# Performance work log

Measured on AMD Instinct MI355X. Metric: run time of the kernel, lower is better.

## Reference

```python
import jax, jax.numpy as jnp
import numpy as np

N_GRAPH = 1024
NODES_PER_GRAPH = 512
TOTAL_NODES = N_GRAPH * NODES_PER_GRAPH  # 524288
D_FEAT = 128
EPS = 1e-06


def setup_inputs() -> dict:
    key = jax.random.key(0)
    k1, k2, k3, k4 = jax.random.split(key, 4)
    x = jax.random.normal(k1, (TOTAL_NODES, D_FEAT), dtype=jnp.float32)
    # per-graph node counts; sum(n_node) == TOTAL_NODES (equal-size graphs)
    n_node = jnp.full((N_GRAPH,), NODES_PER_GRAPH, dtype=jnp.int32)
    mean_scale = jax.random.uniform(k2, (D_FEAT,), dtype=jnp.float32)
    scale = jax.random.uniform(k3, (D_FEAT,), dtype=jnp.float32)
    bias = jax.random.normal(k4, (D_FEAT,), dtype=jnp.float32)
    return {"x": x, "n_node": n_node, "mean_scale": mean_scale, "scale": scale, "bias": bias}


def reference(x, n_node, mean_scale, scale, bias):
    n_graph = n_node.shape[0]
    total_nodes = x.shape[0]
    node_graph_idx = jnp.repeat(jnp.arange(n_graph), n_node, axis=0,
                                total_repeat_length=total_nodes)  # [N]
    ones = jnp.ones((total_nodes, 1), dtype=x.dtype)
    counts = jax.ops.segment_sum(ones, node_graph_idx, n_graph)  # [G,1]
    # per-graph mean, broadcast back to nodes
    mean_g = jax.ops.segment_sum(x, node_graph_idx, n_graph) / counts  # [G,D]
    mean_n = jnp.repeat(mean_g, n_node, axis=0, total_repeat_length=total_nodes)
    # NOTE: faithful to source - the mean is scaled by mean_scale BEFORE both
    # the centering and the variance computation.
    mean_n = mean_n * mean_scale
    y = x - mean_n
    var_g = jax.ops.segment_sum((x - mean_n) ** 2, node_graph_idx, n_graph) / counts
    var_n = jnp.repeat(var_g, n_node, axis=0, total_repeat_length=total_nodes)
    mul = jax.lax.rsqrt(var_n + EPS) * scale
    y = y * mul + bias
    return y.astype(x.dtype)
```

## Files before the change

kernel.cpp:

```cpp
#include <hip/hip_runtime.h>

#define D_FEAT 128
#define F4 (D_FEAT / 4)
#define BLOCK 1024
#define FAST_NODES 512
#define PER_THREAD (FAST_NODES * F4 / BLOCK)
#define EPS 1e-6f

__global__ __launch_bounds__(BLOCK, 4) void graphnorm_kernel(
    const float* __restrict__ x,
    const int* __restrict__ n_node,
    const float* __restrict__ mean_scale,
    const float* __restrict__ scale,
    const float* __restrict__ bias,
    float* __restrict__ y,
    int n_graph)
{
    const int g    = blockIdx.x;
    const int t    = threadIdx.x;
    const int lane = t & 63;
    const int wave = t >> 6;
    const int grp  = t & 31;
    const int nsub = t >> 5;

    __shared__ int    s_int[16];
    __shared__ float4 s_sum[16][32];
    __shared__ float4 s_sq [16][32];
    __shared__ float4 s_a[32];
    __shared__ float4 s_b[32];
    __shared__ int    s_off;

    int my = 0;
    for (int i = t; i < g; i += BLOCK) my += n_node[i];
    #pragma unroll
    for (int o = 32; o; o >>= 1) my += __shfl_down(my, o);
    if (lane == 0) s_int[wave] = my;
    __syncthreads();
    if (t == 0) {
        int tot = 0;
        #pragma unroll
        for (int w = 0; w < 16; w++) tot += s_int[w];
        s_off = tot;
    }
    __syncthreads();
    const int   node0 = s_off;
    const int   cnt   = n_node[g];
    const float inv   = 1.0f / (float)cnt;

    const float4* __restrict__ xg = (const float4*)x + (size_t)node0 * F4;
    float4*       __restrict__ yg = (float4*)y       + (size_t)node0 * F4;

    float4 sum = make_float4(0.f, 0.f, 0.f, 0.f);
    float4 sq  = make_float4(0.f, 0.f, 0.f, 0.f);

    float4 v[PER_THREAD];
    const bool fast = (cnt == FAST_NODES);

    if (fast) {
        #pragma unroll
        for (int i = 0; i < PER_THREAD; i++) {
            const int node = nsub + 32 * i;
            v[i] = xg[(size_t)node * F4 + grp];
            sum.x += v[i].x; sum.y += v[i].y; sum.z += v[i].z; sum.w += v[i].w;
            sq.x  += v[i].x * v[i].x; sq.y += v[i].y * v[i].y;
            sq.z  += v[i].z * v[i].z; sq.w += v[i].w * v[i].w;
        }
    } else {
        for (int node = nsub; node < cnt; node += 32) {
            float4 val = xg[(size_t)node * F4 + grp];
            sum.x += val.x; sum.y += val.y; sum.z += val.z; sum.w += val.w;
            sq.x  += val.x * val.x; sq.y += val.y * val.y;
            sq.z  += val.z * val.z; sq.w += val.w * val.w;
        }
    }

    sum.x += __shfl_down(sum.x, 32); sum.y += __shfl_down(sum.y, 32);
    sum.z += __shfl_down(sum.z, 32); sum.w += __shfl_down(sum.w, 32);
    sq.x  += __shfl_down(sq.x, 32);  sq.y  += __shfl_down(sq.y, 32);
    sq.z  += __shfl_down(sq.z, 32);  sq.w  += __shfl_down(sq.w, 32);
    if (lane < 32) { s_sum[wave][lane] = sum; s_sq[wave][lane] = sq; }
    __syncthreads();

    if (t < 32) {
        float4 S = make_float4(0.f, 0.f, 0.f, 0.f);
        float4 Q = make_float4(0.f, 0.f, 0.f, 0.f);
        #pragma unroll
        for (int w = 0; w < 16; w++) {
            float4 a4 = s_sum[w][t];
            float4 b4 = s_sq[w][t];
            S.x += a4.x; S.y += a4.y; S.z += a4.z; S.w += a4.w;
            Q.x += b4.x; Q.y += b4.y; Q.z += b4.z; Q.w += b4.w;
        }
        const float4 ms = ((const float4*)mean_scale)[t];
        const float4 sc = ((const float4*)scale)[t];
        const float4 bs = ((const float4*)bias)[t];

        float4 A, B;
        {
            float mean = S.x * inv, m = mean * ms.x;
            float var  = Q.x * inv - 2.f * m * mean + m * m;
            A.x = rsqrtf(var + EPS) * sc.x; B.x = bs.x - m * A.x;
        }
        {
            float mean = S.y * inv, m = mean * ms.y;
            float var  = Q.y * inv - 2.f * m * mean + m * m;
            A.y = rsqrtf(var + EPS) * sc.y; B.y = bs.y - m * A.y;
        }
        {
            float mean = S.z * inv, m = mean * ms.z;
            float var  = Q.z * inv - 2.f * m * mean + m * m;
            A.z = rsqrtf(var + EPS) * sc.z; B.z = bs.z - m * A.z;
        }
        {
            float mean = S.w * inv, m = mean * ms.w;
            float var  = Q.w * inv - 2.f * m * mean + m * m;
            A.w = rsqrtf(var + EPS) * sc.w; B.w = bs.w - m * A.w;
        }
        s_a[t] = A; s_b[t] = B;
    }
    __syncthreads();

    const float4 a = s_a[grp];
    const float4 b = s_b[grp];

    if (fast) {
        #pragma unroll
        for (int i = 0; i < PER_THREAD; i++) {
            const int node = nsub + 32 * i;
            float4 r;
            r.x = v[i].x * a.x + b.x;
            r.y = v[i].y * a.y + b.y;
            r.z = v[i].z * a.z + b.z;
            r.w = v[i].w * a.w + b.w;
            yg[(size_t)node * F4 + grp] = r;
        }
    } else {
        for (int node = nsub; node < cnt; node += 32) {
            float4 val = xg[(size_t)node * F4 + grp];
            float4 r;
            r.x = val.x * a.x + b.x;
            r.y = val.y * a.y + b.y;
            r.z = val.z * a.z + b.z;
            r.w = val.w * a.w + b.w;
            yg[(size_t)node * F4 + grp] = r;
        }
    }
}

extern "C" void kernel_launch(void* const* d_in, const int* in_sizes, int n_in,
                              void* d_out, int out_size, void* d_ws, size_t ws_size,
                              hipStream_t stream) {
    const float* x          = (const float*)d_in[0];
    const int*   n_node     = (const int*)d_in[1];
    const float* mean_scale = (const float*)d_in[2];
    const float* scale      = (const float*)d_in[3];
    const float* bias       = (const float*)d_in[4];
    float*       y          = (float*)d_out;

    const int n_graph = in_sizes[1];

    graphnorm_kernel<<<n_graph, BLOCK, 0, stream>>>(
        x, n_node, mean_scale, scale, bias, y, n_graph);
}
```

Before: 452.6 us.

## Split graph norm into separate stats and apply kernels with reverse-order apply

Replaces the single fused kernel, which held each graph's rows in registers, with a stats kernel that computes per-graph scale and shift and an apply kernel that rereads x. Both use 512-thread blocks with higher occupancy, and the apply pass walks graphs in reverse so recently read data may still be in cache. Coefficients go to workspace, or into the output buffer when no workspace is given. The cost is a second full read of x plus an extra launch.

```diff
diff --git a/kernel.cpp b/kernel.cpp
--- a/kernel.cpp
+++ b/kernel.cpp
@@ -1,91 +1,94 @@
 #include <hip/hip_runtime.h>
 
 #define D_FEAT 128
-#define F4 (D_FEAT / 4)
-#define BLOCK 1024
-#define FAST_NODES 512
-#define PER_THREAD (FAST_NODES * F4 / BLOCK)
-#define EPS 1e-6f
-
-__global__ __launch_bounds__(BLOCK, 4) void graphnorm_kernel(
-    const float* __restrict__ x,
-    const int* __restrict__ n_node,
-    const float* __restrict__ mean_scale,
-    const float* __restrict__ scale,
-    const float* __restrict__ bias,
-    float* __restrict__ y,
-    int n_graph)
+#define F4     (D_FEAT / 4)
+#define BLOCK  512
+#define EPS    1e-6f
+
+__device__ __forceinline__ int graph_offset(const int* __restrict__ n_node,
+                                            int g, int t)
 {
-    const int g    = blockIdx.x;
-    const int t    = threadIdx.x;
-    const int lane = t & 63;
-    const int wave = t >> 6;
-    const int grp  = t & 31;
-    const int nsub = t >> 5;
-
-    __shared__ int    s_int[16];
-    __shared__ float4 s_sum[16][32];
-    __shared__ float4 s_sq [16][32];
-    __shared__ float4 s_a[32];
-    __shared__ float4 s_b[32];
-    __shared__ int    s_off;
-
+    __shared__ int s_red[8];
+    __shared__ int s_off;
     int my = 0;
     for (int i = t; i < g; i += BLOCK) my += n_node[i];
     #pragma unroll
     for (int o = 32; o; o >>= 1) my += __shfl_down(my, o);
-    if (lane == 0) s_int[wave] = my;
+    if ((t & 63) == 0) s_red[t >> 6] = my;
     __syncthreads();
     if (t == 0) {
         int tot = 0;
         #pragma unroll
-        for (int w = 0; w < 16; w++) tot += s_int[w];
+        for (int w = 0; w < 8; w++) tot += s_red[w];
         s_off = tot;
     }
     __syncthreads();
-    const int   node0 = s_off;
-    const int   cnt   = n_node[g];
-    const float inv   = 1.0f / (float)cnt;
+    return s_off;
+}
+
+__global__ __launch_bounds__(BLOCK, 8) void gn_stats(
+    const float* __restrict__ x,
+    const int*   __restrict__ n_node,
+    const float* __restrict__ mean_scale,
+    const float* __restrict__ scale,
+    const float* __restrict__ bias,
+    float*       __restrict__ y,
+    float4*      __restrict__ coef,
+    int n_graph, int mode)
+{
+    const int g    = blockIdx.x;
+    const int t    = threadIdx.x;
+    const int grp  = t & 31;
+    const int nsub = t >> 5;
+    const int wave = t >> 6;
+    const int lane = t & 63;
+
+    const int node0 = graph_offset(n_node, g, t);
+    const int cnt   = n_node[g];
 
     const float4* __restrict__ xg = (const float4*)x + (size_t)node0 * F4;
-    float4*       __restrict__ yg = (float4*)y       + (size_t)node0 * F4;
 
     float4 sum = make_float4(0.f, 0.f, 0.f, 0.f);
     float4 sq  = make_float4(0.f, 0.f, 0.f, 0.f);
 
-    float4 v[PER_THREAD];
-    const bool fast = (cnt == FAST_NODES);
-
-    if (fast) {
-        #pragma unroll
-        for (int i = 0; i < PER_THREAD; i++) {
-            const int node = nsub + 32 * i;
-            v[i] = xg[(size_t)node * F4 + grp];
-            sum.x += v[i].x; sum.y += v[i].y; sum.z += v[i].z; sum.w += v[i].w;
-            sq.x  += v[i].x * v[i].x; sq.y += v[i].y * v[i].y;
-            sq.z  += v[i].z * v[i].z; sq.w += v[i].w * v[i].w;
-        }
-    } else {
-        for (int node = nsub; node < cnt; node += 32) {
-            float4 val = xg[(size_t)node * F4 + grp];
-            sum.x += val.x; sum.y += val.y; sum.z += val.z; sum.w += val.w;
-            sq.x  += val.x * val.x; sq.y += val.y * val.y;
-            sq.z  += val.z * val.z; sq.w += val.w * val.w;
-        }
+    int node = nsub;
+    for (; node + 48 < cnt; node += 64) {
+        float4 v0 = xg[(size_t)(node     ) * F4 + grp];
+        float4 v1 = xg[(size_t)(node + 16) * F4 + grp];
+        float4 v2 = xg[(size_t)(node + 32) * F4 + grp];
+        float4 v3 = xg[(size_t)(node + 48) * F4 + grp];
+        sum.x += v0.x + v1.x + v2.x + v3.x;
+        sum.y += v0.y + v1.y + v2.y + v3.y;
+        sum.z += v0.z + v1.z + v2.z + v3.z;
+        sum.w += v0.w + v1.w + v2.w + v3.w;
+        sq.x += v0.x*v0.x + v1.x*v1.x + v2.x*v2.x + v3.x*v3.x;
+        sq.y += v0.y*v0.y + v1.y*v1.y + v2.y*v2.y + v3.y*v3.y;
+        sq.z += v0.z*v0.z + v1.z*v1.z + v2.z*v2.z + v3.z*v3.z;
+        sq.w += v0.w*v0.w + v1.w*v1.w + v2.w*v2.w + v3.w*v3.w;
+    }
+    for (; node < cnt; node += 16) {
+        float4 v0 = xg[(size_t)node * F4 + grp];
+        sum.x += v0.x; sum.y += v0.y; sum.z += v0.z; sum.w += v0.w;
+        sq.x += v0.x*v0.x; sq.y += v0.y*v0.y;
+        sq.z += v0.z*v0.z; sq.w += v0.w*v0.w;
     }
 
     sum.x += __shfl_down(sum.x, 32); sum.y += __shfl_down(sum.y, 32);
     sum.z += __shfl_down(sum.z, 32); sum.w += __shfl_down(sum.w, 32);
     sq.x  += __shfl_down(sq.x, 32);  sq.y  += __shfl_down(sq.y, 32);
     sq.z  += __shfl_down(sq.z, 32);  sq.w  += __shfl_down(sq.w, 32);
+
+    __shared__ float4 s_sum[8][32];
+    __shared__ float4 s_sq [8][32];
     if (lane < 32) { s_sum[wave][lane] = sum; s_sq[wave][lane] = sq; }
     __syncthreads();
 
     if (t < 32) {
+        const float inv = 1.0f / (float)cnt;
         float4 S = make_float4(0.f, 0.f, 0.f, 0.f);
         float4 Q = make_float4(0.f, 0.f, 0.f, 0.f);
         #pragma unroll
-        for (int w = 0; w < 16; w++) {
+        for (int w = 0; w < 8; w++) {
             float4 a4 = s_sum[w][t];
             float4 b4 = s_sq[w][t];
             S.x += a4.x; S.y += a4.y; S.z += a4.z; S.w += a4.w;
@@ -116,34 +119,79 @@
             float var  = Q.w * inv - 2.f * m * mean + m * m;
             A.w = rsqrtf(var + EPS) * sc.w; B.w = bs.w - m * A.w;
         }
-        s_a[t] = A; s_b[t] = B;
+
+        if (mode == 0) {
+            coef[(size_t)g * 32 + t]             = A;
+            coef[(size_t)(n_graph + g) * 32 + t] = B;
+        } else if (cnt >= 2) {
+            float4* ygc = (float4*)y + (size_t)node0 * F4;
+            ygc[t]      = A;
+            ygc[32 + t] = B;
+        }
+    }
+}
+
+__global__ __launch_bounds__(BLOCK, 8) void gn_apply(
+    const float* __restrict__ x,
+    const int*   __restrict__ n_node,
+    float*       __restrict__ y,
+    const float4* __restrict__ coef,
+    int n_graph, int mode)
+{
+    const int g    = n_graph - 1 - blockIdx.x;
+    const int t    = threadIdx.x;
+    const int grp  = t & 31;
+    const int nsub = t >> 5;
+
+    const int node0 = graph_offset(n_node, g, t);
+    const int cnt   = n_node[g];
+
+    __shared__ float4 s_a[32];
+    __shared__ float4 s_b[32];
+    if (mode == 0) {
+        if (t < 32)      s_a[t]      = coef[(size_t)g * 32 + t];
+        else if (t < 64) s_b[t - 32] = coef[(size_t)(n_graph + g) * 32 + (t - 32)];
+    } else {
+        const float4* ygc = (const float4*)y + (size_t)node0 * F4;
+        if (t < 64) {
+            if (t < 32) s_a[t]      = ygc[t];
+            else        s_b[t - 32] = ygc[t];
+        }
     }
     __syncthreads();
 
     const float4 a = s_a[grp];
     const float4 b = s_b[grp];
 
-    if (fast) {
-        #pragma unroll
-        for (int i = 0; i < PER_THREAD; i++) {
-            const int node = nsub + 32 * i;
-            float4 r;
-            r.x = v[i].x * a.x + b.x;
-            r.y = v[i].y * a.y + b.y;
-            r.z = v[i].z * a.z + b.z;
-            r.w = v[i].w * a.w + b.w;
-            yg[(size_t)node * F4 + grp] = r;
-        }
-    } else {
-        for (int node = nsub; node < cnt; node += 32) {
-            float4 val = xg[(size_t)node * F4 + grp];
-            float4 r;
-            r.x = val.x * a.x + b.x;
-            r.y = val.y * a.y + b.y;
-            r.z = val.z * a.z + b.z;
-            r.w = val.w * a.w + b.w;
-            yg[(size_t)node * F4 + grp] = r;
-        }
+    const float4* __restrict__ xg = (const float4*)x + (size_t)node0 * F4;
+    float4*       __restrict__ yg = (float4*)y       + (size_t)node0 * F4;
+
+    int node = nsub;
+    for (; node + 48 < cnt; node += 64) {
+        float4 v0 = xg[(size_t)(node     ) * F4 + grp];
+        float4 v1 = xg[(size_t)(node + 16) * F4 + grp];
+        float4 v2 = xg[(size_t)(node + 32) * F4 + grp];
+        float4 v3 = xg[(size_t)(node + 48) * F4 + grp];
+        float4 r0, r1, r2, r3;
+        r0.x = fmaf(v0.x, a.x, b.x); r0.y = fmaf(v0.y, a.y, b.y);
+        r0.z = fmaf(v0.z, a.z, b.z); r0.w = fmaf(v0.w, a.w, b.w);
+        r1.x = fmaf(v1.x, a.x, b.x); r1.y = fmaf(v1.y, a.y, b.y);
+        r1.z = fmaf(v1.z, a.z, b.z); r1.w = fmaf(v1.w, a.w, b.w);
+        r2.x = fmaf(v2.x, a.x, b.x); r2.y = fmaf(v2.y, a.y, b.y);
+        r2.z = fmaf(v2.z, a.z, b.z); r2.w = fmaf(v2.w, a.w, b.w);
+        r3.x = fmaf(v3.x, a.x, b.x); r3.y = fmaf(v3.y, a.y, b.y);
+        r3.z = fmaf(v3.z, a.z, b.z); r3.w = fmaf(v3.w, a.w, b.w);
+        yg[(size_t)(node     ) * F4 + grp] = r0;
+        yg[(size_t)(node + 16) * F4 + grp] = r1;
+        yg[(size_t)(node + 32) * F4 + grp] = r2;
+        yg[(size_t)(node + 48) * F4 + grp] = r3;
+    }
+    for (; node < cnt; node += 16) {
+        float4 v0 = xg[(size_t)node * F4 + grp];
+        float4 r0;
+        r0.x = fmaf(v0.x, a.x, b.x); r0.y = fmaf(v0.y, a.y, b.y);
+        r0.z = fmaf(v0.z, a.z, b.z); r0.w = fmaf(v0.w, a.w, b.w);
+        yg[(size_t)node * F4 + grp] = r0;
     }
 }
 
@@ -159,6 +207,13 @@
 
     const int n_graph = in_sizes[1];
 
-    graphnorm_kernel<<<n_graph, BLOCK, 0, stream>>>(
-        x, n_node, mean_scale, scale, bias, y, n_graph);
-}
+    const size_t need = (size_t)n_graph * D_FEAT * 2 * sizeof(float);
+    int     mode = 1;
+    float4* coef = nullptr;
+    if (d_ws != nullptr && ws_size >= need) { mode = 0; coef = (float4*)d_ws; }
+
+    gn_stats<<<n_graph, BLOCK, 0, stream>>>(
+        x, n_node, mean_scale, scale, bias, y, coef, n_graph, mode);
+    gn_apply<<<n_graph, BLOCK, 0, stream>>>(
+        x, n_node, y, coef, n_graph, mode);
+}
```

Result: slower. 523.2 us (+15.6%).

## Make graphnorm persistent with software-pipelined store of previous graph

Applied to the files above, without the earlier changes.

Replaces the one-block-per-graph launch with a persistent grid of 256 blocks that loop over graphs in a strided order, keeping a running node offset. Inside each iteration, the normalized stores for the previous graph are interleaved with the loads for the next graph, so reads and writes overlap instead of alternating per block. This cuts block launch overhead and tail effects. In exchange it adds per-iteration prefix sums and barriers, and the 256-block grid may leave some CUs with fewer resident waves.

```diff
diff --git a/kernel.cpp b/kernel.cpp
--- a/kernel.cpp
+++ b/kernel.cpp
@@ -1,78 +1,46 @@
 #include <hip/hip_runtime.h>
 
 #define D_FEAT 128
-#define F4 (D_FEAT / 4)
-#define BLOCK 1024
+#define F4     (D_FEAT / 4)
+#define BLOCK  1024
+#define GRID   256
 #define FAST_NODES 512
-#define PER_THREAD (FAST_NODES * F4 / BLOCK)
-#define EPS 1e-6f
-
-__global__ __launch_bounds__(BLOCK, 4) void graphnorm_kernel(
-    const float* __restrict__ x,
-    const int* __restrict__ n_node,
-    const float* __restrict__ mean_scale,
-    const float* __restrict__ scale,
-    const float* __restrict__ bias,
-    float* __restrict__ y,
-    int n_graph)
+#define PT     (FAST_NODES * F4 / BLOCK)
+#define EPS    1e-6f
+
+__device__ __forceinline__ int coop_sum(const int* __restrict__ n_node,
+                                        int lo, int hi, int t)
 {
-    const int g    = blockIdx.x;
-    const int t    = threadIdx.x;
-    const int lane = t & 63;
-    const int wave = t >> 6;
-    const int grp  = t & 31;
-    const int nsub = t >> 5;
-
-    __shared__ int    s_int[16];
+    __shared__ int s_red[16];
+    __shared__ int s_tot;
+    int my = 0;
+    for (int i = lo + t; i < hi; i += BLOCK) my += n_node[i];
+    #pragma unroll
+    for (int o = 32; o; o >>= 1) my += __shfl_down(my, o);
+    if ((t & 63) == 0) s_red[t >> 6] = my;
+    __syncthreads();
+    if (t == 0) {
+        int tot = 0;
+        #pragma unroll
+        for (int w = 0; w < 16; w++) tot += s_red[w];
+        s_tot = tot;
+    }
+    __syncthreads();
+    return s_tot;
+}
+
+__device__ __forceinline__ void reduce_coef(
+    float4 sum, float4 sq, float inv,
+    const float4* __restrict__ ms4,
+    const float4* __restrict__ sc4,
+    const float4* __restrict__ bs4,
+    int t, float4& a_out, float4& b_out)
+{
     __shared__ float4 s_sum[16][32];
     __shared__ float4 s_sq [16][32];
     __shared__ float4 s_a[32];
     __shared__ float4 s_b[32];
-    __shared__ int    s_off;
-
-    int my = 0;
-    for (int i = t; i < g; i += BLOCK) my += n_node[i];
-    #pragma unroll
-    for (int o = 32; o; o >>= 1) my += __shfl_down(my, o);
-    if (lane == 0) s_int[wave] = my;
-    __syncthreads();
-    if (t == 0) {
-        int tot = 0;
-        #pragma unroll
-        for (int w = 0; w < 16; w++) tot += s_int[w];
-        s_off = tot;
-    }
-    __syncthreads();
-    const int   node0 = s_off;
-    const int   cnt   = n_node[g];
-    const float inv   = 1.0f / (float)cnt;
-
-    const float4* __restrict__ xg = (const float4*)x + (size_t)node0 * F4;
-    float4*       __restrict__ yg = (float4*)y       + (size_t)node0 * F4;
-
-    float4 sum = make_float4(0.f, 0.f, 0.f, 0.f);
-    float4 sq  = make_float4(0.f, 0.f, 0.f, 0.f);
-
-    float4 v[PER_THREAD];
-    const bool fast = (cnt == FAST_NODES);
-
-    if (fast) {
-        #pragma unroll
-        for (int i = 0; i < PER_THREAD; i++) {
-            const int node = nsub + 32 * i;
-            v[i] = xg[(size_t)node * F4 + grp];
-            sum.x += v[i].x; sum.y += v[i].y; sum.z += v[i].z; sum.w += v[i].w;
-            sq.x  += v[i].x * v[i].x; sq.y += v[i].y * v[i].y;
-            sq.z  += v[i].z * v[i].z; sq.w += v[i].w * v[i].w;
-        }
-    } else {
-        for (int node = nsub; node < cnt; node += 32) {
-            float4 val = xg[(size_t)node * F4 + grp];
-            sum.x += val.x; sum.y += val.y; sum.z += val.z; sum.w += val.w;
-            sq.x  += val.x * val.x; sq.y += val.y * val.y;
-            sq.z  += val.z * val.z; sq.w += val.w * val.w;
-        }
-    }
+    const int wave = t >> 6, lane = t & 63, grp = t & 31;
 
     sum.x += __shfl_down(sum.x, 32); sum.y += __shfl_down(sum.y, 32);
     sum.z += __shfl_down(sum.z, 32); sum.w += __shfl_down(sum.w, 32);
@@ -91,10 +59,9 @@
             S.x += a4.x; S.y += a4.y; S.z += a4.z; S.w += a4.w;
             Q.x += b4.x; Q.y += b4.y; Q.z += b4.z; Q.w += b4.w;
         }
-        const float4 ms = ((const float4*)mean_scale)[t];
-        const float4 sc = ((const float4*)scale)[t];
-        const float4 bs = ((const float4*)bias)[t];
-
+        const float4 ms = ms4[t];
+        const float4 sc = sc4[t];
+        const float4 bs = bs4[t];
         float4 A, B;
         {
             float mean = S.x * inv, m = mean * ms.x;
@@ -119,30 +86,128 @@
         s_a[t] = A; s_b[t] = B;
     }
     __syncthreads();
-
-    const float4 a = s_a[grp];
-    const float4 b = s_b[grp];
-
-    if (fast) {
+    a_out = s_a[grp];
+    b_out = s_b[grp];
+}
+
+__global__ __launch_bounds__(BLOCK, 4) void graphnorm_persist(
+    const float* __restrict__ x,
+    const int*   __restrict__ n_node,
+    const float* __restrict__ mean_scale,
+    const float* __restrict__ scale,
+    const float* __restrict__ bias,
+    float*       __restrict__ y,
+    int n_graph)
+{
+    const int t    = threadIdx.x;
+    const int grp  = t & 31;
+    const int nsub = t >> 5;
+    const int nb   = gridDim.x;
+
+    const float4* ms4 = (const float4*)mean_scale;
+    const float4* sc4 = (const float4*)scale;
+    const float4* bs4 = (const float4*)bias;
+
+    int g = blockIdx.x;
+    if (g >= n_graph) return;
+    int node0 = coop_sum(n_node, 0, g, t);
+
+    float4 v[PT];
+    float4 a_p, b_p;
+    float4* yg_p = nullptr;
+    int pend = 0;
+
+    for (;;) {
+        const int   cnt = n_node[g];
+        const float inv = 1.0f / (float)cnt;
+        const float4* __restrict__ xg = (const float4*)x + (size_t)node0 * F4;
+        float4*       __restrict__ yg = (float4*)y       + (size_t)node0 * F4;
+
+        if (cnt == FAST_NODES) {
+            float4 sum = make_float4(0.f, 0.f, 0.f, 0.f);
+            float4 sq  = make_float4(0.f, 0.f, 0.f, 0.f);
+            if (pend) {
+                #pragma unroll
+                for (int i = 0; i < PT; i++) {
+                    const size_t idx = (size_t)(nsub + 32 * i) * F4 + grp;
+                    float4 r;
+                    r.x = fmaf(v[i].x, a_p.x, b_p.x);
+                    r.y = fmaf(v[i].y, a_p.y, b_p.y);
+                    r.z = fmaf(v[i].z, a_p.z, b_p.z);
+                    r.w = fmaf(v[i].w, a_p.w, b_p.w);
+                    yg_p[idx] = r;
+                    float4 nv = xg[idx];
+                    sum.x += nv.x; sum.y += nv.y; sum.z += nv.z; sum.w += nv.w;
+                    sq.x  += nv.x * nv.x; sq.y += nv.y * nv.y;
+                    sq.z  += nv.z * nv.z; sq.w += nv.w * nv.w;
+                    v[i] = nv;
+                }
+            } else {
+                #pragma unroll
+                for (int i = 0; i < PT; i++) {
+                    const size_t idx = (size_t)(nsub + 32 * i) * F4 + grp;
+                    float4 nv = xg[idx];
+                    sum.x += nv.x; sum.y += nv.y; sum.z += nv.z; sum.w += nv.w;
+                    sq.x  += nv.x * nv.x; sq.y += nv.y * nv.y;
+                    sq.z  += nv.z * nv.z; sq.w += nv.w * nv.w;
+                    v[i] = nv;
+                }
+            }
+            reduce_coef(sum, sq, inv, ms4, sc4, bs4, t, a_p, b_p);
+            yg_p = yg;
+            pend = 1;
+        } else {
+            if (pend) {
+                #pragma unroll
+                for (int i = 0; i < PT; i++) {
+                    const size_t idx = (size_t)(nsub + 32 * i) * F4 + grp;
+                    float4 r;
+                    r.x = fmaf(v[i].x, a_p.x, b_p.x);
+                    r.y = fmaf(v[i].y, a_p.y, b_p.y);
+                    r.z = fmaf(v[i].z, a_p.z, b_p.z);
+                    r.w = fmaf(v[i].w, a_p.w, b_p.w);
+                    yg_p[idx] = r;
+                }
+                pend = 0;
+            }
+            float4 sum = make_float4(0.f, 0.f, 0.f, 0.f);
+            float4 sq  = make_float4(0.f, 0.f, 0.f, 0.f);
+            for (int node = nsub; node < cnt; node += 32) {
+                float4 nv = xg[(size_t)node * F4 + grp];
+                sum.x += nv.x; sum.y += nv.y; sum.z += nv.z; sum.w += nv.w;
+                sq.x  += nv.x * nv.x; sq.y += nv.y * nv.y;
+                sq.z  += nv.z * nv.z; sq.w += nv.w * nv.w;
+            }
+            float4 a, b;
+            reduce_coef(sum, sq, inv, ms4, sc4, bs4, t, a, b);
+            for (int node = nsub; node < cnt; node += 32) {
+                const size_t idx = (size_t)node * F4 + grp;
+                float4 nv = xg[idx];
+                float4 r;
+                r.x = fmaf(nv.x, a.x, b.x);
+                r.y = fmaf(nv.y, a.y, b.y);
+                r.z = fmaf(nv.z, a.z, b.z);
+                r.w = fmaf(nv.w, a.w, b.w);
+                yg[idx] = r;
+            }
+        }
+
+        const int next = g + nb;
+        if (next >= n_graph) break;
+        node0 += coop_sum(n_node, g, next, t);
+        g = next;
+    }
+
+    if (pend) {
         #pragma unroll
-        for (int i = 0; i < PER_THREAD; i++) {
-            const int node = nsub + 32 * i;
+        for (int i = 0; i < PT; i++) {
+            const size_t idx = (size_t)(nsub + 32 * i) * F4 + grp;
             float4 r;
-            r.x = v[i].x * a.x + b.x;
-            r.y = v[i].y * a.y + b.y;
-            r.z = v[i].z * a.z + b.z;
-            r.w = v[i].w * a.w + b.w;
-            yg[(size_t)node * F4 + grp] = r;
-        }
-    } else {
-        for (int node = nsub; node < cnt; node += 32) {
-            float4 val = xg[(size_t)node * F4 + grp];
-            float4 r;
-            r.x = val.x * a.x + b.x;
-            r.y = val.y * a.y + b.y;
-            r.z = val.z * a.z + b.z;
-            r.w = val.w * a.w + b.w;
-            yg[(size_t)node * F4 + grp] = r;
+            r.x = fmaf(v[i].x, a_p.x, b_p.x);
+            r.y = fmaf(v[i].y, a_p.y, b_p.y);
+            r.z = fmaf(v[i].z, a_p.z, b_p.z);
+            r.w = fmaf(v[i].w, a_p.w, b_p.w);
+            yg_p[idx] = r;
         }
     }
 }
@@ -158,7 +223,8 @@
     float*       y          = (float*)d_out;
 
     const int n_graph = in_sizes[1];
-
-    graphnorm_kernel<<<n_graph, BLOCK, 0, stream>>>(
+    const int grid    = (n_graph < GRID) ? n_graph : GRID;
+
+    graphnorm_persist<<<grid, BLOCK, 0, stream>>>(
         x, n_node, mean_scale, scale, bias, y, n_graph);
 }
```

Measured after the change: 475.0 us. 5.0% more time.

## Split each graph's feature dimension across two blocks of 512 threads

Applied to the files above, without the earlier changes.

Each graph is now handled by two blocks, each covering half of the 128 features, with 512 threads per block instead of 1024. This gives twice as many smaller blocks, aiming for better load balance and occupancy on a memory-bound kernel. Each block recomputes the graph offset prefix sum. Rows are fetched in 256-byte halves by separate blocks, which could reduce access efficiency.

```diff
diff --git a/kernel.cpp b/kernel.cpp
--- a/kernel.cpp
+++ b/kernel.cpp
@@ -1,100 +1,71 @@
 #include <hip/hip_runtime.h>
 
 #define D_FEAT 128
-#define F4 (D_FEAT / 4)
-#define BLOCK 1024
+#define F4ALL  (D_FEAT / 4)
+#define F4H    (F4ALL / 2)
+#define BLOCK  512
 #define FAST_NODES 512
-#define PER_THREAD (FAST_NODES * F4 / BLOCK)
-#define EPS 1e-6f
+#define PT     16
+#define EPS    1e-6f
 
-__global__ __launch_bounds__(BLOCK, 4) void graphnorm_kernel(
-    const float* __restrict__ x,
-    const int* __restrict__ n_node,
-    const float* __restrict__ mean_scale,
-    const float* __restrict__ scale,
-    const float* __restrict__ bias,
-    float* __restrict__ y,
-    int n_graph)
+__device__ __forceinline__ int graph_offset(const int* __restrict__ n_node,
+                                            int g, int t)
 {
-    const int g    = blockIdx.x;
-    const int t    = threadIdx.x;
-    const int lane = t & 63;
-    const int wave = t >> 6;
-    const int grp  = t & 31;
-    const int nsub = t >> 5;
-
-    __shared__ int    s_int[16];
-    __shared__ float4 s_sum[16][32];
-    __shared__ float4 s_sq [16][32];
-    __shared__ float4 s_a[32];
-    __shared__ float4 s_b[32];
-    __shared__ int    s_off;
-
+    __shared__ int s_red[8];
+    __shared__ int s_off;
     int my = 0;
     for (int i = t; i < g; i += BLOCK) my += n_node[i];
     #pragma unroll
     for (int o = 32; o; o >>= 1) my += __shfl_down(my, o);
-    if (lane == 0) s_int[wave] = my;
+    if ((t & 63) == 0) s_red[t >> 6] = my;
     __syncthreads();
     if (t == 0) {
         int tot = 0;
         #pragma unroll
-        for (int w = 0; w < 16; w++) tot += s_int[w];
+        for (int w = 0; w < 8; w++) tot += s_red[w];
         s_off = tot;
     }
     __syncthreads();
-    const int   node0 = s_off;
-    const int   cnt   = n_node[g];
-    const float inv   = 1.0f / (float)cnt;
+    return s_off;
+}
 
-    const float4* __restrict__ xg = (const float4*)x + (size_t)node0 * F4;
-    float4*       __restrict__ yg = (float4*)y       + (size_t)node0 * F4;
-
-    float4 sum = make_float4(0.f, 0.f, 0.f, 0.f);
-    float4 sq  = make_float4(0.f, 0.f, 0.f, 0.f);
-
-    float4 v[PER_THREAD];
-    const bool fast = (cnt == FAST_NODES);
-
-    if (fast) {
-        #pragma unroll
-        for (int i = 0; i < PER_THREAD; i++) {
-            const int node = nsub + 32 * i;
-            v[i] = xg[(size_t)node * F4 + grp];
-            sum.x += v[i].x; sum.y += v[i].y; sum.z += v[i].z; sum.w += v[i].w;
-            sq.x  += v[i].x * v[i].x; sq.y += v[i].y * v[i].y;
-            sq.z  += v[i].z * v[i].z; sq.w += v[i].w * v[i].w;
-        }
-    } else {
-        for (int node = nsub; node < cnt; node += 32) {
-            float4 val = xg[(size_t)node * F4 + grp];
-            sum.x += val.x; sum.y += val.y; sum.z += val.z; sum.w += val.w;
-            sq.x  += val.x * val.x; sq.y += val.y * val.y;
-            sq.z  += val.z * val.z; sq.w += val.w * val.w;
-        }
-    }
+__device__ __forceinline__ void reduce_coef(
+    float4 sum, float4 sq, float inv,
+    const float4* __restrict__ ms4,
+    const float4* __restrict__ sc4,
+    const float4* __restrict__ bs4,
+    int t, float4& a_out, float4& b_out)
+{
+    __shared__ float4 s_sum[8][16];
+    __shared__ float4 s_sq [8][16];
+    __shared__ float4 s_a[16];
+    __shared__ float4 s_b[16];
+    const int wave = t >> 6, lane = t & 63, grp = t & 15;
 
     sum.x += __shfl_down(sum.x, 32); sum.y += __shfl_down(sum.y, 32);
     sum.z += __shfl_down(sum.z, 32); sum.w += __shfl_down(sum.w, 32);
     sq.x  += __shfl_down(sq.x, 32);  sq.y  += __shfl_down(sq.y, 32);
     sq.z  += __shfl_down(sq.z, 32);  sq.w  += __shfl_down(sq.w, 32);
-    if (lane < 32) { s_sum[wave][lane] = sum; s_sq[wave][lane] = sq; }
+    sum.x += __shfl_down(sum.x, 16); sum.y += __shfl_down(sum.y, 16);
+    sum.z += __shfl_down(sum.z, 16); sum.w += __shfl_down(sum.w, 16);
+    sq.x  += __shfl_down(sq.x, 16);  sq.y  += __shfl_down(sq.y, 16);
+    sq.z  += __shfl_down(sq.z, 16);  sq.w  += __shfl_down(sq.w, 16);
+    if (lane < 16) { s_sum[wave][lane] = sum; s_sq[wave][lane] = sq; }
     __syncthreads();
 
-    if (t < 32) {
+    if (t < 16) {
         float4 S = make_float4(0.f, 0.f, 0.f, 0.f);
         float4 Q = make_float4(0.f, 0.f, 0.f, 0.f);
         #pragma unroll
-        for (int w = 0; w < 16; w++) {
+        for (int w = 0; w < 8; w++) {
             float4 a4 = s_sum[w][t];
             float4 b4 = s_sq[w][t];
             S.x += a4.x; S.y += a4.y; S.z += a4.z; S.w += a4.w;
             Q.x += b4.x; Q.y += b4.y; Q.z += b4.z; Q.w += b4.w;
         }
-        const float4 ms = ((const float4*)mean_scale)[t];
-        const float4 sc = ((const float4*)scale)[t];
-        const float4 bs = ((const float4*)bias)[t];
-
+        const float4 ms = ms4[t];
+        const float4 sc = sc4[t];
+        const float4 bs = bs4[t];
         float4 A, B;
         {
             float mean = S.x * inv, m = mean * ms.x;
@@ -119,30 +90,83 @@
         s_a[t] = A; s_b[t] = B;
     }
     __syncthreads();
+    a_out = s_a[grp];
+    b_out = s_b[grp];
+}
 
-    const float4 a = s_a[grp];
-    const float4 b = s_b[grp];
+__global__ __launch_bounds__(BLOCK, 4) void gn_half(
+    const float* __restrict__ x,
+    const int*   __restrict__ n_node,
+    const float* __restrict__ mean_scale,
+    const float* __restrict__ scale,
+    const float* __restrict__ bias,
+    float*       __restrict__ y,
+    int n_graph)
+{
+    const int b    = blockIdx.x;
+    const int g    = b >> 1;
+    const int h    = b & 1;
+    const int t    = threadIdx.x;
+    const int grp  = t & 15;
+    const int nsub = t >> 4;
 
-    if (fast) {
+    if (g >= n_graph) return;
+
+    const int node0 = graph_offset(n_node, g, t);
+    const int cnt   = n_node[g];
+    const float inv = 1.0f / (float)cnt;
+
+    const float4* __restrict__ xg = (const float4*)x + (size_t)node0 * F4ALL + h * F4H;
+    float4*       __restrict__ yg = (float4*)y       + (size_t)node0 * F4ALL + h * F4H;
+    const float4* ms4 = (const float4*)mean_scale + h * F4H;
+    const float4* sc4 = (const float4*)scale      + h * F4H;
+    const float4* bs4 = (const float4*)bias       + h * F4H;
+
+    float4 sum = make_float4(0.f, 0.f, 0.f, 0.f);
+    float4 sq  = make_float4(0.f, 0.f, 0.f, 0.f);
+
+    if (cnt == FAST_NODES) {
+        float4 v[PT];
         #pragma unroll
-        for (int i = 0; i < PER_THREAD; i++) {
-            const int node = nsub + 32 * i;
+        for (int i = 0; i < PT; i++) {
+            const size_t idx = (size_t)(nsub + 32 * i) * F4ALL + grp;
+            v[i] = xg[idx];
+            sum.x += v[i].x; sum.y += v[i].y; sum.z += v[i].z; sum.w += v[i].w;
+            sq.x  += v[i].x * v[i].x; sq.y += v[i].y * v[i].y;
+            sq.z  += v[i].z * v[i].z; sq.w += v[i].w * v[i].w;
+        }
+
+        float4 a, b;
+        reduce_coef(sum, sq, inv, ms4, sc4, bs4, t, a, b);
+
+        #pragma unroll
+        for (int i = 0; i < PT; i++) {
+            const size_t idx = (size_t)(nsub + 32 * i) * F4ALL + grp;
             float4 r;
-            r.x = v[i].x * a.x + b.x;
-            r.y = v[i].y * a.y + b.y;
-            r.z = v[i].z * a.z + b.z;
-            r.w = v[i].w * a.w + b.w;
-            yg[(size_t)node * F4 + grp] = r;
+            r.x = fmaf(v[i].x, a.x, b.x);
+            r.y = fmaf(v[i].y, a.y, b.y);
+            r.z = fmaf(v[i].z, a.z, b.z);
+            r.w = fmaf(v[i].w, a.w, b.w);
+            yg[idx] = r;
         }
     } else {
         for (int node = nsub; node < cnt; node += 32) {
-            float4 val = xg[(size_t)node * F4 + grp];
+            float4 nv = xg[(size_t)node * F4ALL + grp];
+            sum.x += nv.x; sum.y += nv.y; sum.z += nv.z; sum.w += nv.w;
+            sq.x  += nv.x * nv.x; sq.y += nv.y * nv.y;
+            sq.z  += nv.z * nv.z; sq.w += nv.w * nv.w;
+        }
+        float4 a, b;
+        reduce_coef(sum, sq, inv, ms4, sc4, bs4, t, a, b);
+        for (int node = nsub; node < cnt; node += 32) {
+            const size_t idx = (size_t)node * F4ALL + grp;
+            float4 nv = xg[idx];
             float4 r;
-            r.x = val.x * a.x + b.x;
-            r.y = val.y * a.y + b.y;
-            r.z = val.z * a.z + b.z;
-            r.w = val.w * a.w + b.w;
-            yg[(size_t)node * F4 + grp] = r;
+            r.x = fmaf(nv.x, a.x, b.x);
+            r.y = fmaf(nv.y, a.y, b.y);
+            r.z = fmaf(nv.z, a.z, b.z);
+            r.w = fmaf(nv.w, a.w, b.w);
+            yg[idx] = r;
         }
     }
 }
@@ -159,6 +183,6 @@
 
     const int n_graph = in_sizes[1];
 
-    graphnorm_kernel<<<n_graph, BLOCK, 0, stream>>>(
+    gn_half<<<2 * n_graph, BLOCK, 0, stream>>>(
         x, n_node, mean_scale, scale, bias, y, n_graph);
 }
```

Result: faster. 443.5 us (-2.0%).
